# Performance work log

Measured on AMD Instinct MI355X. Metric: run time of the kernel, lower is better.

Reference implementation:

```python
import jax, jax.numpy as jnp
import numpy as np

MAX_STEPS = 32
EPSILON = 0.01
LN_EPS = 1e-5


def setup_inputs() -> dict:
    key = jax.random.key(0)
    ks = jax.random.split(key, 8)
    B, D, H = 4096, 512, 2048
    std = 0.02  # larger than torch init so the loop does not trivially converge
    return {
        "z_init": jax.random.normal(ks[0], (B, D), jnp.float32),
        "ln1_g": jnp.ones((D,), jnp.float32),
        "ln1_b": jnp.zeros((D,), jnp.float32),
        "w1": jax.random.normal(ks[1], (D, H), jnp.float32) * std,
        "b1": jnp.zeros((H,), jnp.float32),
        "w2": jax.random.normal(ks[2], (H, D), jnp.float32) * std,
        "b2": jnp.zeros((D,), jnp.float32),
        "ln2_g": jnp.ones((D,), jnp.float32),
        "ln2_b": jnp.zeros((D,), jnp.float32),
        "w3": jax.random.normal(ks[3], (D, H), jnp.float32) * std,
        "b3": jnp.zeros((H,), jnp.float32),
        "w4": jax.random.normal(ks[4], (H, D), jnp.float32) * std,
        "b4": jnp.zeros((D,), jnp.float32),
        "clf_w": jax.random.normal(ks[5], (D, 1), jnp.float32) * 0.02,
        "clf_b": jnp.zeros((1,), jnp.float32),
    }


def _layernorm(x, g, b):
    m = jnp.mean(x, axis=-1, keepdims=True)
    v = jnp.var(x, axis=-1, keepdims=True)
    return (x - m) * jax.lax.rsqrt(v + LN_EPS) * g + b


def reference(z_init, ln1_g, ln1_b, w1, b1, w2, b2, ln2_g, ln2_b, w3, b3, w4, b4,
              clf_w, clf_b):
    def block(z):
        h = _layernorm(z, ln1_g, ln1_b)
        h = jax.nn.gelu(h @ w1 + b1, approximate=False)
        h = h @ w2 + b2
        h = _layernorm(h, ln2_g, ln2_b)
        h = jax.nn.gelu(h @ w3 + b3, approximate=False)
        return h @ w4 + b4

    def step(carry, _):
        z_t, mask = carry
        delta = block(z_t)                       # [B, D]
        z_next = z_t + delta
        dist = jnp.linalg.norm(delta, axis=-1)   # ||z_next - z_t||_2
        mask = mask | (dist < EPSILON)
        z_t = jnp.where(mask[:, None], z_t, z_next)
        return (z_t, mask), None

    B = z_init.shape[0]
    init = (z_init, jnp.zeros((B,), jnp.bool_))
    (z_t, converged_mask), _ = jax.lax.scan(step, init, None, length=MAX_STEPS)
    logits = z_t @ clf_w + clf_b                 # [B, 1]
    return logits, converged_mask, z_t
```

## Files before the change

kernel.cpp:

```cpp
#include <hip/hip_runtime.h>

#define B_ROWS  4096
#define D_DIM   512
#define H_DIM   2048
#define N_STEPS 32
#define EPS_CONV 0.01f
#define LN_EPSF  1e-5f

typedef __attribute__((ext_vector_type(4))) float f32x4;
typedef __attribute__((ext_vector_type(8))) _Float16 h16x8;
typedef unsigned short ushort_t;
typedef unsigned int uint32;

__device__ __forceinline__ float wave_reduce_sum(float v) {
#pragma unroll
  for (int o = 32; o > 0; o >>= 1) v += __shfl_down(v, o, 64);
  return v;
}

__device__ __forceinline__ float gelu_exact(float v) {
  return 0.5f * v * (1.0f + erff(v * 0.7071067811865476f));
}

__device__ __forceinline__ void async_copy16(void* lds, const void* g) {
  __builtin_amdgcn_global_load_lds(
      (const __attribute__((address_space(1))) unsigned int*)g,
      (__attribute__((address_space(3))) unsigned int*)lds, 16, 0, 0);
}

__device__ __forceinline__ ushort_t h_bits(_Float16 h) {
  union { _Float16 f; ushort_t u; } c; c.f = h; return c.u;
}

__device__ __forceinline__ uint32 pack_split(float v) {
  const _Float16 hi = (_Float16)v;
  const _Float16 lo = (_Float16)((v - (float)hi) * 1024.0f);
  union { _Float16 f[2]; uint32 u; } c;
  c.f[0] = hi; c.f[1] = lo;
  return c.u;
}

__global__ __launch_bounds__(256)
void ln_pack_kernel(const float* in, const float* in2, const float* g,
                    const float* b, uint32* outp) {
  const int row = blockIdx.x;
  const int t = threadIdx.x;
  float2 v = ((const float2*)(in + (size_t)row * D_DIM))[t];
  if (in2 != nullptr) {
    const float2 w = ((const float2*)(in2 + (size_t)row * D_DIM))[t];
    v.x += w.x; v.y += w.y;
  }
  float s  = v.x + v.y;
  float sq = v.x * v.x + v.y * v.y;
  s  = wave_reduce_sum(s);
  sq = wave_reduce_sum(sq);
  __shared__ float sd1[4], sd2[4], mb[2];
  const int lane = t & 63, wid = t >> 6;
  if (lane == 0) { sd1[wid] = s; sd2[wid] = sq; }
  __syncthreads();
  if (t == 0) {
    float st = sd1[0] + sd1[1] + sd1[2] + sd1[3];
    float qt = sd2[0] + sd2[1] + sd2[2] + sd2[3];
    float mean = st * (1.0f / (float)D_DIM);
    float var  = qt * (1.0f / (float)D_DIM) - mean * mean;
    mb[0] = mean;
    mb[1] = rsqrtf(var + LN_EPSF);
  }
  __syncthreads();
  const float mean = mb[0], rstd = mb[1];
  const float2 gv = ((const float2*)g)[t];
  const float2 bv = ((const float2*)b)[t];
  uint2 o;
  o.x = pack_split((v.x - mean) * rstd * gv.x + bv.x);
  o.y = pack_split((v.y - mean) * rstd * gv.y + bv.y);
  ((uint2*)(outp + (size_t)row * D_DIM))[t] = o;
}

__global__ __launch_bounds__(256)
void transpose_split_kernel(const float* __restrict__ w,
                            ushort_t* __restrict__ wh, ushort_t* __restrict__ wl,
                            int K, int N) {
  __shared__ float t[32][33];
  const int tx = threadIdx.x;
  const int ty = threadIdx.y;
  const int n_base = blockIdx.x * 32;
  const int k_base = blockIdx.y * 32;
#pragma unroll
  for (int r = 0; r < 4; ++r)
    t[ty + r * 8][tx] = w[(size_t)(k_base + ty + r * 8) * N + n_base + tx];
  __syncthreads();
#pragma unroll
  for (int r = 0; r < 4; ++r) {
    const int n = n_base + ty + r * 8;
    const int k = k_base + tx;
    const float v = t[tx][ty + r * 8];
    const _Float16 hi = (_Float16)v;
    const _Float16 lo = (_Float16)((v - (float)hi) * 1024.0f);
    wh[(size_t)n * K + k] = h_bits(hi);
    wl[(size_t)n * K + k] = h_bits(lo);
  }
}

template <int BN, bool OUT_PACK>
__global__ __launch_bounds__(256, 2)
void gemm_f16x3p(const uint32* __restrict__ Ap, const ushort_t* __restrict__ Wh,
                 const ushort_t* __restrict__ Wl, const float* __restrict__ bias,
                 uint32* __restrict__ Cp, float* __restrict__ C0,
                 float* __restrict__ C1, int M, int N, int K, int kc) {
  constexpr int BM = 128, BK = 32;
  constexpr int FN = BN / 32;
  constexpr int WR = (BN * 4) / 256;

  __shared__ uint32   As[BM * BK];
  __shared__ ushort_t Bh[BN * BK];
  __shared__ ushort_t Bl[BN * BK];

  const int tid = threadIdx.x;
  const int lane = tid & 63;
  const int wid = tid >> 6;
  const int q = lane >> 4;
  const int l16 = lane & 15;
  const int wm = wid >> 1;
  const int wn = wid & 1;

  const int m0 = blockIdx.x * BM;
  const int n0 = blockIdx.y * BN;
  const int kz = blockIdx.z * kc;

  f32x4 acc_h[4][FN], acc_m[4][FN];
#pragma unroll
  for (int i = 0; i < 4; ++i)
#pragma unroll
    for (int j = 0; j < FN; ++j) {
      acc_h[i][j] = (f32x4){0.f, 0.f, 0.f, 0.f};
      acc_m[i][j] = (f32x4){0.f, 0.f, 0.f, 0.f};
    }

  int a_goff[4];
#pragma unroll
  for (int r = 0; r < 4; ++r) {
    const int p = r * 256 + tid;
    const int am = p >> 3;
    const int ac = ((p & 7) ^ (am & 7)) * 4;
    a_goff[r] = (m0 + am) * K + ac;
  }
  int w_goff[WR];
#pragma unroll
  for (int r = 0; r < WR; ++r) {
    const int p = r * 256 + tid;
    const int n = p >> 2;
    const int cw = ((p & 3) ^ ((n >> 1) & 3)) * 8;
    w_goff[r] = (n0 + n) * K + cw;
  }

  for (int k0 = kz; k0 < kz + kc; k0 += BK) {
#pragma unroll
    for (int r = 0; r < 4; ++r)
      async_copy16(&As[(r * 256 + tid) * 4], &Ap[a_goff[r] + k0]);
#pragma unroll
    for (int r = 0; r < WR; ++r) {
      async_copy16(&Bh[(r * 256 + tid) * 8], &Wh[w_goff[r] + k0]);
      async_copy16(&Bl[(r * 256 + tid) * 8], &Wl[w_goff[r] + k0]);
    }
    __syncthreads();

    h16x8 ah[4], al[4];
#pragma unroll
    for (int i = 0; i < 4; ++i) {
      const int r = wm * 64 + i * 16 + l16;
      const uint4 c0 = *(const uint4*)&As[r * 32 + (((2 * q) + 0) ^ (r & 7)) * 4];
      const uint4 c1 = *(const uint4*)&As[r * 32 + (((2 * q) + 1) ^ (r & 7)) * 4];
      union { uint32 u[4]; h16x8 h; } hu, lu;
      hu.u[0] = __builtin_amdgcn_perm(c0.y, c0.x, 0x05040100u);
      hu.u[1] = __builtin_amdgcn_perm(c0.w, c0.z, 0x05040100u);
      hu.u[2] = __builtin_amdgcn_perm(c1.y, c1.x, 0x05040100u);
      hu.u[3] = __builtin_amdgcn_perm(c1.w, c1.z, 0x05040100u);
      lu.u[0] = __builtin_amdgcn_perm(c0.y, c0.x, 0x07060302u);
      lu.u[1] = __builtin_amdgcn_perm(c0.w, c0.z, 0x07060302u);
      lu.u[2] = __builtin_amdgcn_perm(c1.y, c1.x, 0x07060302u);
      lu.u[3] = __builtin_amdgcn_perm(c1.w, c1.z, 0x07060302u);
      ah[i] = hu.h; al[i] = lu.h;
    }
    h16x8 bh[FN], bl[FN];
#pragma unroll
    for (int j = 0; j < FN; ++j) {
      const int n = wn * (BN / 2) + j * 16 + l16;
      const int off = n * 32 + (q ^ ((n >> 1) & 3)) * 8;
      bh[j] = *(const h16x8*)&Bh[off];
      bl[j] = *(const h16x8*)&Bl[off];
    }
#pragma unroll
    for (int i = 0; i < 4; ++i)
#pragma unroll
      for (int j = 0; j < FN; ++j) {
        acc_h[i][j] = __builtin_amdgcn_mfma_f32_16x16x32_f16(ah[i], bh[j], acc_h[i][j], 0, 0, 0);
        acc_m[i][j] = __builtin_amdgcn_mfma_f32_16x16x32_f16(al[i], bh[j], acc_m[i][j], 0, 0, 0);
        acc_m[i][j] = __builtin_amdgcn_mfma_f32_16x16x32_f16(ah[i], bl[j], acc_m[i][j], 0, 0, 0);
      }
    __syncthreads();
  }

#pragma unroll
  for (int i = 0; i < 4; ++i) {
    const int row = m0 + wm * 64 + i * 16 + q * 4;
#pragma unroll
    for (int j = 0; j < FN; ++j) {
      const int col = n0 + wn * (BN / 2) + j * 16 + l16;
      if (OUT_PACK) {
        const float bv = bias[col];
#pragma unroll
        for (int r = 0; r < 4; ++r) {
          float v = acc_h[i][j][r] + acc_m[i][j][r] * (1.0f / 1024.0f) + bv;
          Cp[(size_t)(row + r) * N + col] = pack_split(gelu_exact(v));
        }
      } else {
        float* C = (blockIdx.z == 0) ? C0 : C1;
        const float bv = (blockIdx.z == 0) ? bias[col] : 0.0f;
#pragma unroll
        for (int r = 0; r < 4; ++r) {
          C[(size_t)(row + r) * N + col] =
              acc_h[i][j][r] + acc_m[i][j][r] * (1.0f / 1024.0f) + bv;
        }
      }
    }
  }
}

__global__ __launch_bounds__(256)
void update_kernel(float* __restrict__ z, const float* __restrict__ d0,
                   const float* __restrict__ d1, int* __restrict__ mask) {
  const int row = blockIdx.x;
  const int t = threadIdx.x;
  float2 d = ((const float2*)(d0 + (size_t)row * D_DIM))[t];
  const float2 e = ((const float2*)(d1 + (size_t)row * D_DIM))[t];
  d.x += e.x; d.y += e.y;
  float sq = d.x * d.x + d.y * d.y;
  sq = wave_reduce_sum(sq);
  __shared__ float sd[4];
  __shared__ int frozen_sh;
  const int lane = t & 63, wid = t >> 6;
  if (lane == 0) sd[wid] = sq;
  __syncthreads();
  if (t == 0) {
    const float dist = sqrtf(sd[0] + sd[1] + sd[2] + sd[3]);
    const int m = mask[row];
    const int newly = (dist < EPS_CONV) ? 1 : 0;
    if (!m && newly) mask[row] = 1;
    frozen_sh = m | newly;
  }
  __syncthreads();
  if (!frozen_sh) {
    float2* zp = (float2*)(z + (size_t)row * D_DIM);
    float2 zv = zp[t];
    zv.x += d.x; zv.y += d.y;
    zp[t] = zv;
  }
}

__global__ __launch_bounds__(256)
void final_kernel(const float* __restrict__ z, const float* __restrict__ clf_w,
                  const float* __restrict__ clf_b, const int* __restrict__ mask,
                  float* __restrict__ logits, float* __restrict__ maskf) {
  const int row = blockIdx.x;
  const int t = threadIdx.x;
  const float2 zv = ((const float2*)(z + (size_t)row * D_DIM))[t];
  const float2 wv = ((const float2*)clf_w)[t];
  float s = zv.x * wv.x + zv.y * wv.y;
  s = wave_reduce_sum(s);
  __shared__ float sd[4];
  const int lane = t & 63, wid = t >> 6;
  if (lane == 0) sd[wid] = s;
  __syncthreads();
  if (t == 0) {
    logits[row] = sd[0] + sd[1] + sd[2] + sd[3] + clf_b[0];
    maskf[row] = mask[row] ? 1.0f : 0.0f;
  }
}

__global__ void init_kernel(const float* __restrict__ z_init,
                            float* __restrict__ z, int* __restrict__ mask,
                            int n) {
  const int i = blockIdx.x * blockDim.x + threadIdx.x;
  if (i < n) z[i] = z_init[i];
  if (i < B_ROWS) mask[i] = 0;
}

__global__ __launch_bounds__(256)
void ln_f32_kernel(const float* __restrict__ in, const float* __restrict__ g,
                   const float* __restrict__ b, float* __restrict__ out) {
  const int row = blockIdx.x;
  const int t = threadIdx.x;
  const float2 v = ((const float2*)(in + (size_t)row * D_DIM))[t];
  float s = v.x + v.y, sq = v.x * v.x + v.y * v.y;
  s = wave_reduce_sum(s); sq = wave_reduce_sum(sq);
  __shared__ float sd1[4], sd2[4], mb[2];
  const int lane = t & 63, wid = t >> 6;
  if (lane == 0) { sd1[wid] = s; sd2[wid] = sq; }
  __syncthreads();
  if (t == 0) {
    float st = sd1[0] + sd1[1] + sd1[2] + sd1[3];
    float qt = sd2[0] + sd2[1] + sd2[2] + sd2[3];
    float mean = st / (float)D_DIM;
    float var = qt / (float)D_DIM - mean * mean;
    mb[0] = mean; mb[1] = rsqrtf(var + LN_EPSF);
  }
  __syncthreads();
  const float mean = mb[0], rstd = mb[1];
  const float2 gv = ((const float2*)g)[t];
  const float2 bv = ((const float2*)b)[t];
  float2 r;
  r.x = (v.x - mean) * rstd * gv.x + bv.x;
  r.y = (v.y - mean) * rstd * gv.y + bv.y;
  ((float2*)(out + (size_t)row * D_DIM))[t] = r;
}

__global__ __launch_bounds__(256)
void update_f32_kernel(float* __restrict__ z, const float* __restrict__ delta,
                       int* __restrict__ mask) {
  const int row = blockIdx.x;
  const int t = threadIdx.x;
  const float2 d = ((const float2*)(delta + (size_t)row * D_DIM))[t];
  float sq = d.x * d.x + d.y * d.y;
  sq = wave_reduce_sum(sq);
  __shared__ float sd[4];
  __shared__ int frozen_sh;
  const int lane = t & 63, wid = t >> 6;
  if (lane == 0) sd[wid] = sq;
  __syncthreads();
  if (t == 0) {
    const float dist = sqrtf(sd[0] + sd[1] + sd[2] + sd[3]);
    const int m = mask[row];
    const int newly = (dist < EPS_CONV) ? 1 : 0;
    if (!m && newly) mask[row] = 1;
    frozen_sh = m | newly;
  }
  __syncthreads();
  if (!frozen_sh) {
    float2* zp = (float2*)(z + (size_t)row * D_DIM);
    float2 zv = zp[t];
    zv.x += d.x; zv.y += d.y;
    zp[t] = zv;
  }
}

template <int BM, int BN>
__global__ __launch_bounds__(256)
void gemm_fp32_fallback(const float* __restrict__ A, const float* __restrict__ W,
                        const float* __restrict__ bias, float* __restrict__ C,
                        int M, int N, int K, int do_gelu) {
  constexpr int BK = 8;
  constexpr int TM = BM / 16;
  constexpr int TN = BN / 16;
  __shared__ float As[BK][BM];
  __shared__ float Bs[BK][BN];
  const int tid = threadIdx.x;
  const int m0 = blockIdx.x * BM;
  const int n0 = blockIdx.y * BN;
  const int ty = tid >> 4, tx = tid & 15;
  float acc[TM][TN];
#pragma unroll
  for (int i = 0; i < TM; ++i)
#pragma unroll
    for (int j = 0; j < TN; ++j) acc[i][j] = 0.0f;
  for (int k0 = 0; k0 < K; k0 += BK) {
    if constexpr (BM == 128) {
      const int row = tid >> 1, col = (tid & 1) * 4;
      const float4 a = *(const float4*)(A + (size_t)(m0 + row) * K + k0 + col);
      As[col + 0][row] = a.x; As[col + 1][row] = a.y;
      As[col + 2][row] = a.z; As[col + 3][row] = a.w;
    } else {
      const int row = tid >> 2, col = (tid & 3) * 2;
      const float2 a = *(const float2*)(A + (size_t)(m0 + row) * K + k0 + col);
      As[col + 0][row] = a.x; As[col + 1][row] = a.y;
    }
    {
      const int row = tid >> 5, col = (tid & 31) * 4;
      const float4 w = *(const float4*)(W + (size_t)(k0 + row) * N + n0 + col);
      *(float4*)(&Bs[row][col]) = w;
    }
    __syncthreads();
#pragma unroll
    for (int kk = 0; kk < BK; ++kk) {
      float a[TM], b[TN];
#pragma unroll
      for (int i = 0; i < TM; i += 4)
        *(float4*)(a + i) = *(const float4*)(&As[kk][ty * TM + i]);
#pragma unroll
      for (int j = 0; j < TN; j += 4)
        *(float4*)(b + j) = *(const float4*)(&Bs[kk][tx * TN + j]);
#pragma unroll
      for (int i = 0; i < TM; ++i)
#pragma unroll
        for (int j = 0; j < TN; ++j) acc[i][j] = fmaf(a[i], b[j], acc[i][j]);
    }
    __syncthreads();
  }
  float bv[TN];
#pragma unroll
  for (int j = 0; j < TN; ++j) bv[j] = bias[n0 + tx * TN + j];
#pragma unroll
  for (int i = 0; i < TM; ++i) {
    const int r = m0 + ty * TM + i;
#pragma unroll
    for (int j = 0; j < TN; j += 4) {
      float4 v;
      v.x = acc[i][j + 0] + bv[j + 0]; v.y = acc[i][j + 1] + bv[j + 1];
      v.z = acc[i][j + 2] + bv[j + 2]; v.w = acc[i][j + 3] + bv[j + 3];
      if (do_gelu) {
        v.x = gelu_exact(v.x); v.y = gelu_exact(v.y);
        v.z = gelu_exact(v.z); v.w = gelu_exact(v.w);
      }
      *(float4*)(C + (size_t)r * N + n0 + tx * TN + j) = v;
    }
  }
}

extern "C" void kernel_launch(void* const* d_in, const int* in_sizes, int n_in,
                              void* d_out, int out_size, void* d_ws,
                              size_t ws_size, hipStream_t stream) {
  const float* z_init = (const float*)d_in[0];
  const float* ln1_g  = (const float*)d_in[1];
  const float* ln1_b  = (const float*)d_in[2];
  const float* w1     = (const float*)d_in[3];
  const float* b1     = (const float*)d_in[4];
  const float* w2     = (const float*)d_in[5];
  const float* b2     = (const float*)d_in[6];
  const float* ln2_g  = (const float*)d_in[7];
  const float* ln2_b  = (const float*)d_in[8];
  const float* w3     = (const float*)d_in[9];
  const float* b3     = (const float*)d_in[10];
  const float* w4     = (const float*)d_in[11];
  const float* b4     = (const float*)d_in[12];
  const float* clf_w  = (const float*)d_in[13];
  const float* clf_b  = (const float*)d_in[14];

  float* out    = (float*)d_out;
  float* logits = out;
  float* maskf  = out + B_ROWS;
  float* z      = out + 2 * B_ROWS;

  const size_t BD = (size_t)B_ROWS * D_DIM;
  const size_t BH = (size_t)B_ROWS * H_DIM;
  const size_t WSZ = (size_t)D_DIM * H_DIM;

  uint32* xp = (uint32*)d_ws;
  uint32* hp = xp + BD;
  float*  y  = (float*)(hp + BH);
  ushort_t* wt = (ushort_t*)(y + BD);
  ushort_t* w1h = wt + 0 * WSZ; ushort_t* w1l = wt + 1 * WSZ;
  ushort_t* w2h = wt + 2 * WSZ; ushort_t* w2l = wt + 3 * WSZ;
  ushort_t* w3h = wt + 4 * WSZ; ushort_t* w3l = wt + 5 * WSZ;
  ushort_t* w4h = wt + 6 * WSZ; ushort_t* w4l = wt + 7 * WSZ;
  int* mask = (int*)(wt + 8 * WSZ);
  float* p1 = (float*)xp;
  const size_t need = BD * 4 + BH * 4 + BD * 4 + 8 * WSZ * 2 + B_ROWS * 4 + 256;

  init_kernel<<<(int)((BD + 255) / 256), 256, 0, stream>>>(z_init, z, mask,
                                                           (int)BD);

  if (ws_size >= need) {
    const dim3 tb(32, 8);
    transpose_split_kernel<<<dim3(H_DIM / 32, D_DIM / 32), tb, 0, stream>>>(w1, w1h, w1l, D_DIM, H_DIM);
    transpose_split_kernel<<<dim3(D_DIM / 32, H_DIM / 32), tb, 0, stream>>>(w2, w2h, w2l, H_DIM, D_DIM);
    transpose_split_kernel<<<dim3(H_DIM / 32, D_DIM / 32), tb, 0, stream>>>(w3, w3h, w3l, D_DIM, H_DIM);
    transpose_split_kernel<<<dim3(D_DIM / 32, H_DIM / 32), tb, 0, stream>>>(w4, w4h, w4l, H_DIM, D_DIM);

    const dim3 g_up(B_ROWS / 128, H_DIM / 128, 1);
    const dim3 g_dn(B_ROWS / 128, D_DIM / 64, 2);
    for (int s = 0; s < N_STEPS; ++s) {
      ln_pack_kernel<<<B_ROWS, 256, 0, stream>>>(z, nullptr, ln1_g, ln1_b, xp);
      gemm_f16x3p<128, true><<<g_up, 256, 0, stream>>>(
          xp, w1h, w1l, b1, hp, nullptr, nullptr, B_ROWS, H_DIM, D_DIM, D_DIM);
      gemm_f16x3p<64, false><<<g_dn, 256, 0, stream>>>(
          hp, w2h, w2l, b2, nullptr, y, p1, B_ROWS, D_DIM, H_DIM, H_DIM / 2);
      ln_pack_kernel<<<B_ROWS, 256, 0, stream>>>(y, p1, ln2_g, ln2_b, xp);
      gemm_f16x3p<128, true><<<g_up, 256, 0, stream>>>(
          xp, w3h, w3l, b3, hp, nullptr, nullptr, B_ROWS, H_DIM, D_DIM, D_DIM);
      gemm_f16x3p<64, false><<<g_dn, 256, 0, stream>>>(
          hp, w4h, w4l, b4, nullptr, y, p1, B_ROWS, D_DIM, H_DIM, H_DIM / 2);
      update_kernel<<<B_ROWS, 256, 0, stream>>>(z, y, p1, mask);
    }
  } else {
    float* x  = (float*)d_ws;
    float* yf = x + BD;
    float* h  = yf + BD;
    int* mask_fb = (int*)(h + BH);
    mask = mask_fb;
    const dim3 g_up(B_ROWS / 128, H_DIM / 128);
    const dim3 g_dn(B_ROWS / 64, D_DIM / 128);
    for (int s = 0; s < N_STEPS; ++s) {
      ln_f32_kernel<<<B_ROWS, 256, 0, stream>>>(z, ln1_g, ln1_b, x);
      gemm_fp32_fallback<128, 128><<<g_up, 256, 0, stream>>>(x, w1, b1, h, B_ROWS, H_DIM, D_DIM, 1);
      gemm_fp32_fallback<64, 128><<<g_dn, 256, 0, stream>>>(h, w2, b2, yf, B_ROWS, D_DIM, H_DIM, 0);
      ln_f32_kernel<<<B_ROWS, 256, 0, stream>>>(yf, ln2_g, ln2_b, x);
      gemm_fp32_fallback<128, 128><<<g_up, 256, 0, stream>>>(x, w3, b3, h, B_ROWS, H_DIM, D_DIM, 1);
      gemm_fp32_fallback<64, 128><<<g_dn, 256, 0, stream>>>(h, w4, b4, yf, B_ROWS, D_DIM, H_DIM, 0);
      update_f32_kernel<<<B_ROWS, 256, 0, stream>>>(z, yf, mask);
    }
  }
  final_kernel<<<B_ROWS, 256, 0, stream>>>(z, clf_w, clf_b, mask, logits, maskf);
}
```

Baseline: 5.199 ms.

## Pre-tile operands into MFMA fragment layout and load directly from global

Activations and weights are stored in a blocked 16x32 fragment layout with hi/lo halves packed together, so each lane's MFMA operands are contiguous 32-byte loads. The GEMM drops LDS staging and block barriers and reads fragments straight from global memory into registers. This removes LDS traffic and synchronisation but gives up cross-wave reuse through shared memory and has no software prefetch, increasing reliance on L2/L1 bandwidth and exposing load latency.

```diff
diff --git a/kernel.cpp b/kernel.cpp
--- a/kernel.cpp
+++ b/kernel.cpp
@@ -22,22 +22,17 @@
   return 0.5f * v * (1.0f + erff(v * 0.7071067811865476f));
 }
 
-__device__ __forceinline__ void async_copy16(void* lds, const void* g) {
-  __builtin_amdgcn_global_load_lds(
-      (const __attribute__((address_space(1))) unsigned int*)g,
-      (__attribute__((address_space(3))) unsigned int*)lds, 16, 0, 0);
-}
-
-__device__ __forceinline__ ushort_t h_bits(_Float16 h) {
-  union { _Float16 f; ushort_t u; } c; c.f = h; return c.u;
-}
-
 __device__ __forceinline__ uint32 pack_split(float v) {
   const _Float16 hi = (_Float16)v;
   const _Float16 lo = (_Float16)((v - (float)hi) * 1024.0f);
   union { _Float16 f[2]; uint32 u; } c;
   c.f[0] = hi; c.f[1] = lo;
   return c.u;
+}
+
+__device__ __forceinline__ size_t amap(int row, int k, int K) {
+  return ((size_t)((row >> 4) * (K >> 5) + (k >> 5)) << 9) +
+         ((row & 15) << 5) + (((k >> 3) & 3) << 3) + (k & 7);
 }
 
 __global__ __launch_bounds__(256)
@@ -73,13 +68,12 @@
   uint2 o;
   o.x = pack_split((v.x - mean) * rstd * gv.x + bv.x);
   o.y = pack_split((v.y - mean) * rstd * gv.y + bv.y);
-  ((uint2*)(outp + (size_t)row * D_DIM))[t] = o;
+  *(uint2*)(outp + amap(row, 2 * t, D_DIM)) = o;
 }
 
 __global__ __launch_bounds__(256)
 void transpose_split_kernel(const float* __restrict__ w,
-                            ushort_t* __restrict__ wh, ushort_t* __restrict__ wl,
-                            int K, int N) {
+                            uint32* __restrict__ wp, int K, int N) {
   __shared__ float t[32][33];
   const int tx = threadIdx.x;
   const int ty = threadIdx.y;
@@ -93,27 +87,19 @@
   for (int r = 0; r < 4; ++r) {
     const int n = n_base + ty + r * 8;
     const int k = k_base + tx;
-    const float v = t[tx][ty + r * 8];
-    const _Float16 hi = (_Float16)v;
-    const _Float16 lo = (_Float16)((v - (float)hi) * 1024.0f);
-    wh[(size_t)n * K + k] = h_bits(hi);
-    wl[(size_t)n * K + k] = h_bits(lo);
+    wp[amap(n, k, K)] = pack_split(t[tx][ty + r * 8]);
   }
 }
 
 template <int BN, bool OUT_PACK>
 __global__ __launch_bounds__(256, 2)
-void gemm_f16x3p(const uint32* __restrict__ Ap, const ushort_t* __restrict__ Wh,
-                 const ushort_t* __restrict__ Wl, const float* __restrict__ bias,
-                 uint32* __restrict__ Cp, float* __restrict__ C0,
-                 float* __restrict__ C1, int M, int N, int K, int kc) {
-  constexpr int BM = 128, BK = 32;
+void gemm_direct(const uint32* __restrict__ Ap, const uint32* __restrict__ Wp,
+                 const float* __restrict__ bias, uint32* __restrict__ Cp,
+                 float* __restrict__ C0, float* __restrict__ C1,
+                 int M, int N, int K, int kc) {
   constexpr int FN = BN / 32;
-  constexpr int WR = (BN * 4) / 256;
-
-  __shared__ uint32   As[BM * BK];
-  __shared__ ushort_t Bh[BN * BK];
-  __shared__ ushort_t Bl[BN * BK];
+  const int KT = K >> 5;
+  const int NKT = kc >> 5;
 
   const int tid = threadIdx.x;
   const int lane = tid & 63;
@@ -123,9 +109,24 @@
   const int wm = wid >> 1;
   const int wn = wid & 1;
 
-  const int m0 = blockIdx.x * BM;
+  const int m0 = blockIdx.x * 128;
   const int n0 = blockIdx.y * BN;
-  const int kz = blockIdx.z * kc;
+  const int kt0 = blockIdx.z * NKT;
+
+  const int loff = l16 * 32 + q * 8;
+
+  const uint32* pa[4];
+#pragma unroll
+  for (int i = 0; i < 4; ++i) {
+    const int tm = (m0 >> 4) + wm * 4 + i;
+    pa[i] = Ap + ((size_t)(tm * KT + kt0) << 9) + loff;
+  }
+  const uint32* pb[FN];
+#pragma unroll
+  for (int j = 0; j < FN; ++j) {
+    const int tn = (n0 >> 4) + wn * FN + j;
+    pb[j] = Wp + ((size_t)(tn * KT + kt0) << 9) + loff;
+  }
 
   f32x4 acc_h[4][FN], acc_m[4][FN];
 #pragma unroll
@@ -136,58 +137,46 @@
       acc_m[i][j] = (f32x4){0.f, 0.f, 0.f, 0.f};
     }
 
-  int a_goff[4];
-#pragma unroll
-  for (int r = 0; r < 4; ++r) {
-    const int p = r * 256 + tid;
-    const int am = p >> 3;
-    const int ac = ((p & 7) ^ (am & 7)) * 4;
-    a_goff[r] = (m0 + am) * K + ac;
-  }
-  int w_goff[WR];
-#pragma unroll
-  for (int r = 0; r < WR; ++r) {
-    const int p = r * 256 + tid;
-    const int n = p >> 2;
-    const int cw = ((p & 3) ^ ((n >> 1) & 3)) * 8;
-    w_goff[r] = (n0 + n) * K + cw;
-  }
-
-  for (int k0 = kz; k0 < kz + kc; k0 += BK) {
-#pragma unroll
-    for (int r = 0; r < 4; ++r)
-      async_copy16(&As[(r * 256 + tid) * 4], &Ap[a_goff[r] + k0]);
-#pragma unroll
-    for (int r = 0; r < WR; ++r) {
-      async_copy16(&Bh[(r * 256 + tid) * 8], &Wh[w_goff[r] + k0]);
-      async_copy16(&Bl[(r * 256 + tid) * 8], &Wl[w_goff[r] + k0]);
-    }
-    __syncthreads();
-
-    h16x8 ah[4], al[4];
+  for (int kt = 0; kt < NKT; ++kt) {
+    uint4 ca0[4], ca1[4], cb0[FN], cb1[FN];
 #pragma unroll
     for (int i = 0; i < 4; ++i) {
-      const int r = wm * 64 + i * 16 + l16;
-      const uint4 c0 = *(const uint4*)&As[r * 32 + (((2 * q) + 0) ^ (r & 7)) * 4];
-      const uint4 c1 = *(const uint4*)&As[r * 32 + (((2 * q) + 1) ^ (r & 7)) * 4];
+      ca0[i] = *(const uint4*)(pa[i]);
+      ca1[i] = *(const uint4*)(pa[i] + 4);
+      pa[i] += 512;
+    }
+#pragma unroll
+    for (int j = 0; j < FN; ++j) {
+      cb0[j] = *(const uint4*)(pb[j]);
+      cb1[j] = *(const uint4*)(pb[j] + 4);
+      pb[j] += 512;
+    }
+    h16x8 ah[4], al[4], bh[FN], bl[FN];
+#pragma unroll
+    for (int i = 0; i < 4; ++i) {
       union { uint32 u[4]; h16x8 h; } hu, lu;
-      hu.u[0] = __builtin_amdgcn_perm(c0.y, c0.x, 0x05040100u);
-      hu.u[1] = __builtin_amdgcn_perm(c0.w, c0.z, 0x05040100u);
-      hu.u[2] = __builtin_amdgcn_perm(c1.y, c1.x, 0x05040100u);
-      hu.u[3] = __builtin_amdgcn_perm(c1.w, c1.z, 0x05040100u);
-      lu.u[0] = __builtin_amdgcn_perm(c0.y, c0.x, 0x07060302u);
-      lu.u[1] = __builtin_amdgcn_perm(c0.w, c0.z, 0x07060302u);
-      lu.u[2] = __builtin_amdgcn_perm(c1.y, c1.x, 0x07060302u);
-      lu.u[3] = __builtin_amdgcn_perm(c1.w, c1.z, 0x07060302u);
+      hu.u[0] = __builtin_amdgcn_perm(ca0[i].y, ca0[i].x, 0x05040100u);
+      hu.u[1] = __builtin_amdgcn_perm(ca0[i].w, ca0[i].z, 0x05040100u);
+      hu.u[2] = __builtin_amdgcn_perm(ca1[i].y, ca1[i].x, 0x05040100u);
+      hu.u[3] = __builtin_amdgcn_perm(ca1[i].w, ca1[i].z, 0x05040100u);
+      lu.u[0] = __builtin_amdgcn_perm(ca0[i].y, ca0[i].x, 0x07060302u);
+      lu.u[1] = __builtin_amdgcn_perm(ca0[i].w, ca0[i].z, 0x07060302u);
+      lu.u[2] = __builtin_amdgcn_perm(ca1[i].y, ca1[i].x, 0x07060302u);
+      lu.u[3] = __builtin_amdgcn_perm(ca1[i].w, ca1[i].z, 0x07060302u);
       ah[i] = hu.h; al[i] = lu.h;
     }
-    h16x8 bh[FN], bl[FN];
 #pragma unroll
     for (int j = 0; j < FN; ++j) {
-      const int n = wn * (BN / 2) + j * 16 + l16;
-      const int off = n * 32 + (q ^ ((n >> 1) & 3)) * 8;
-      bh[j] = *(const h16x8*)&Bh[off];
-      bl[j] = *(const h16x8*)&Bl[off];
+      union { uint32 u[4]; h16x8 h; } hu, lu;
+      hu.u[0] = __builtin_amdgcn_perm(cb0[j].y, cb0[j].x, 0x05040100u);
+      hu.u[1] = __builtin_amdgcn_perm(cb0[j].w, cb0[j].z, 0x05040100u);
+      hu.u[2] = __builtin_amdgcn_perm(cb1[j].y, cb1[j].x, 0x05040100u);
+      hu.u[3] = __builtin_amdgcn_perm(cb1[j].w, cb1[j].z, 0x05040100u);
+      lu.u[0] = __builtin_amdgcn_perm(cb0[j].y, cb0[j].x, 0x07060302u);
+      lu.u[1] = __builtin_amdgcn_perm(cb0[j].w, cb0[j].z, 0x07060302u);
+      lu.u[2] = __builtin_amdgcn_perm(cb1[j].y, cb1[j].x, 0x07060302u);
+      lu.u[3] = __builtin_amdgcn_perm(cb1[j].w, cb1[j].z, 0x07060302u);
+      bh[j] = hu.h; bl[j] = lu.h;
     }
 #pragma unroll
     for (int i = 0; i < 4; ++i)
@@ -197,7 +186,6 @@
         acc_m[i][j] = __builtin_amdgcn_mfma_f32_16x16x32_f16(al[i], bh[j], acc_m[i][j], 0, 0, 0);
         acc_m[i][j] = __builtin_amdgcn_mfma_f32_16x16x32_f16(ah[i], bl[j], acc_m[i][j], 0, 0, 0);
       }
-    __syncthreads();
   }
 
 #pragma unroll
@@ -211,7 +199,7 @@
 #pragma unroll
         for (int r = 0; r < 4; ++r) {
           float v = acc_h[i][j][r] + acc_m[i][j][r] * (1.0f / 1024.0f) + bv;
-          Cp[(size_t)(row + r) * N + col] = pack_split(gelu_exact(v));
+          Cp[amap(row + r, col, N)] = pack_split(gelu_exact(v));
         }
       } else {
         float* C = (blockIdx.z == 0) ? C0 : C1;
@@ -443,41 +431,40 @@
   const size_t BH = (size_t)B_ROWS * H_DIM;
   const size_t WSZ = (size_t)D_DIM * H_DIM;
 
-  uint32* xp = (uint32*)d_ws;
-  uint32* hp = xp + BD;
-  float*  y  = (float*)(hp + BH);
-  ushort_t* wt = (ushort_t*)(y + BD);
-  ushort_t* w1h = wt + 0 * WSZ; ushort_t* w1l = wt + 1 * WSZ;
-  ushort_t* w2h = wt + 2 * WSZ; ushort_t* w2l = wt + 3 * WSZ;
-  ushort_t* w3h = wt + 4 * WSZ; ushort_t* w3l = wt + 5 * WSZ;
-  ushort_t* w4h = wt + 6 * WSZ; ushort_t* w4l = wt + 7 * WSZ;
-  int* mask = (int*)(wt + 8 * WSZ);
-  float* p1 = (float*)xp;
-  const size_t need = BD * 4 + BH * 4 + BD * 4 + 8 * WSZ * 2 + B_ROWS * 4 + 256;
+  uint32* xp  = (uint32*)d_ws;
+  uint32* hp  = xp + BD;
+  float*  y   = (float*)(hp + BH);
+  uint32* w1p = (uint32*)(y + BD);
+  uint32* w2p = w1p + WSZ;
+  uint32* w3p = w2p + WSZ;
+  uint32* w4p = w3p + WSZ;
+  int*    mask = (int*)(w4p + WSZ);
+  float*  p1  = (float*)(mask + B_ROWS);
+  const size_t need = (uintptr_t)((char*)(p1 + BD) - (char*)d_ws) + 256;
 
   init_kernel<<<(int)((BD + 255) / 256), 256, 0, stream>>>(z_init, z, mask,
                                                            (int)BD);
 
   if (ws_size >= need) {
     const dim3 tb(32, 8);
-    transpose_split_kernel<<<dim3(H_DIM / 32, D_DIM / 32), tb, 0, stream>>>(w1, w1h, w1l, D_DIM, H_DIM);
-    transpose_split_kernel<<<dim3(D_DIM / 32, H_DIM / 32), tb, 0, stream>>>(w2, w2h, w2l, H_DIM, D_DIM);
-    transpose_split_kernel<<<dim3(H_DIM / 32, D_DIM / 32), tb, 0, stream>>>(w3, w3h, w3l, D_DIM, H_DIM);
-    transpose_split_kernel<<<dim3(D_DIM / 32, H_DIM / 32), tb, 0, stream>>>(w4, w4h, w4l, H_DIM, D_DIM);
+    transpose_split_kernel<<<dim3(H_DIM / 32, D_DIM / 32), tb, 0, stream>>>(w1, w1p, D_DIM, H_DIM);
+    transpose_split_kernel<<<dim3(D_DIM / 32, H_DIM / 32), tb, 0, stream>>>(w2, w2p, H_DIM, D_DIM);
+    transpose_split_kernel<<<dim3(H_DIM / 32, D_DIM / 32), tb, 0, stream>>>(w3, w3p, D_DIM, H_DIM);
+    transpose_split_kernel<<<dim3(D_DIM / 32, H_DIM / 32), tb, 0, stream>>>(w4, w4p, H_DIM, D_DIM);
 
     const dim3 g_up(B_ROWS / 128, H_DIM / 128, 1);
     const dim3 g_dn(B_ROWS / 128, D_DIM / 64, 2);
     for (int s = 0; s < N_STEPS; ++s) {
       ln_pack_kernel<<<B_ROWS, 256, 0, stream>>>(z, nullptr, ln1_g, ln1_b, xp);
-      gemm_f16x3p<128, true><<<g_up, 256, 0, stream>>>(
-          xp, w1h, w1l, b1, hp, nullptr, nullptr, B_ROWS, H_DIM, D_DIM, D_DIM);
-      gemm_f16x3p<64, false><<<g_dn, 256, 0, stream>>>(
-          hp, w2h, w2l, b2, nullptr, y, p1, B_ROWS, D_DIM, H_DIM, H_DIM / 2);
+      gemm_direct<128, true><<<g_up, 256, 0, stream>>>(
+          xp, w1p, b1, hp, nullptr, nullptr, B_ROWS, H_DIM, D_DIM, D_DIM);
+      gemm_direct<64, false><<<g_dn, 256, 0, stream>>>(
+          hp, w2p, b2, nullptr, y, p1, B_ROWS, D_DIM, H_DIM, H_DIM / 2);
       ln_pack_kernel<<<B_ROWS, 256, 0, stream>>>(y, p1, ln2_g, ln2_b, xp);
-      gemm_f16x3p<128, true><<<g_up, 256, 0, stream>>>(
-          xp, w3h, w3l, b3, hp, nullptr, nullptr, B_ROWS, H_DIM, D_DIM, D_DIM);
-      gemm_f16x3p<64, false><<<g_dn, 256, 0, stream>>>(
-          hp, w4h, w4l, b4, nullptr, y, p1, B_ROWS, D_DIM, H_DIM, H_DIM / 2);
+      gemm_direct<128, true><<<g_up, 256, 0, stream>>>(
+          xp, w3p, b3, hp, nullptr, nullptr, B_ROWS, H_DIM, D_DIM, D_DIM);
+      gemm_direct<64, false><<<g_dn, 256, 0, stream>>>(
+          hp, w4p, b4, nullptr, y, p1, B_ROWS, D_DIM, H_DIM, H_DIM / 2);
       update_kernel<<<B_ROWS, 256, 0, stream>>>(z, y, p1, mask);
     }
   } else {
```

Result: slower. 10.87 ms (+109.2%).
